# Kernel tuning notes

Measured on AMD Instinct MI355X. Metric: run time of the kernel, lower is better.

## Reference

```python
import jax, jax.numpy as jnp
import numpy as np

N_HEAD = 8


def setup_inputs() -> dict:
    key = jax.random.key(0)
    k1, k2, k3 = jax.random.split(key, 3)
    B, D, L = 4, 1024, 2048  # channels-first: (batch, feature, seq)
    q = jax.random.normal(k1, (B, D, L), dtype=jnp.float32)
    k = jax.random.normal(k2, (B, D, L), dtype=jnp.float32)
    v = jax.random.normal(k3, (B, D, L), dtype=jnp.float32)
    gamma = jnp.ones((), dtype=jnp.float32)  # nn.Parameter scalar, init 1.0
    return {"q": q, "k": k, "v": v, "gamma": gamma}


def reference(q, k, v, gamma):
    # q, k, v: (B, D, L) channels-first. Head split on feature dim (-2).
    B, Dq, Lq = q.shape
    Dv, Lk = v.shape[-2], v.shape[-1]
    h = N_HEAD
    dq = Dq // h  # per-head query/key dim
    dv = Dv // h  # per-head value dim
    qh = q.reshape(B, h, dq, Lq)
    kh = k.reshape(B, h, dq, Lk)
    vh = v.reshape(B, h, dv, Lk)
    # scale = sqrt(q.size(-2)) AFTER head split, i.e. sqrt(d_head)
    scale = 1.0 / jnp.sqrt(jnp.asarray(dq, dtype=q.dtype))
    # qk: (B, h, Lq, Lk)
    qk = jnp.einsum('bhdq,bhdl->bhql', qh, kh) * scale
    sm = jax.nn.softmax(qk, axis=-1)
    # torch: (sm.unsqueeze(-3) * v.unsqueeze(-2)).sum(-1) == contraction over Lk
    ret = jnp.einsum('bhql,bhdl->bhdq', sm, vh)  # (B, h, dv, Lq)
    ret = ret.reshape(B, Dv, Lq)  # torch: ret.view(-1, v_shape[-2], q_shape[-1])
    return gamma * ret
```

## Files before the change

kernel.cpp:

```cpp
#include <hip/hip_runtime.h>

#define SEQ 2048
#define DHEAD 128
#define BK 32
#define NBH 32

typedef __attribute__((ext_vector_type(8))) short bf16x8;
typedef __attribute__((ext_vector_type(4))) float f32x4;

__device__ __forceinline__ unsigned short f2bf(float f) {
    unsigned u = __builtin_bit_cast(unsigned, f);
    u += 0x7fffu + ((u >> 16) & 1u);
    return (unsigned short)(u >> 16);
}

__device__ __forceinline__ void gload16(const unsigned short* g, unsigned short* l) {
    __builtin_amdgcn_global_load_lds((const __attribute__((address_space(1))) void*)g,
                                     (__attribute__((address_space(3))) void*)l, 16, 0, 0);
}

__global__ __launch_bounds__(256)
void cvt_kernel(const float* __restrict__ kin, const float* __restrict__ vin,
                unsigned short* __restrict__ kout, unsigned short* __restrict__ vout) {
    const int tid = threadIdx.x;
    if (blockIdx.x < 1024) {
        __shared__ unsigned short tileT[DHEAD][66];
        const int bh = blockIdx.x & 31;
        const int l0 = (blockIdx.x >> 5) * 64;
        const float* ip = kin + (size_t)bh * DHEAD * SEQ;
        unsigned short* opx = kout + ((size_t)bh * SEQ + l0) * DHEAD;
        const int l4 = (tid & 15) * 4;
        const int dq = tid >> 4;
        for (int pass = 0; pass < 8; ++pass) {
            int d = pass * 16 + dq;
            float4 f = *(const float4*)&ip[(size_t)d * SEQ + l0 + l4];
            unsigned lo = (unsigned)f2bf(f.x) | ((unsigned)f2bf(f.y) << 16);
            unsigned hi = (unsigned)f2bf(f.z) | ((unsigned)f2bf(f.w) << 16);
            *(unsigned*)&tileT[d][l4]     = lo;
            *(unsigned*)&tileT[d][l4 + 2] = hi;
        }
        __syncthreads();
        const int lw = tid >> 2;
        const int cw = tid & 3;
        for (int j = 0; j < 4; ++j) {
            int pc = j * 4 + cw;
            int lc = pc ^ (lw & 7);
            unsigned short tmp[8];
            for (int k2 = 0; k2 < 8; ++k2) tmp[k2] = tileT[lc * 8 + k2][lw];
            *(bf16x8*)&opx[(size_t)lw * DHEAD + pc * 8] = *(bf16x8*)tmp;
        }
    } else {
        size_t f = ((size_t)(blockIdx.x - 1024) * 256 + tid) * 8;
        int bh  = (int)(f >> 18);
        int rem = (int)(f & 262143);
        int kt  = rem >> 12;
        int r2  = rem & 4095;
        int dv  = r2 >> 5;
        int e0  = r2 & 31;
        const float* src = vin + ((size_t)bh * DHEAD + dv) * SEQ + kt * BK + e0;
        float4 a = *(const float4*)src;
        float4 b = *(const float4*)(src + 4);
        unsigned short r[8] = {f2bf(a.x), f2bf(a.y), f2bf(a.z), f2bf(a.w),
                               f2bf(b.x), f2bf(b.y), f2bf(b.z), f2bf(b.w)};
        int pc = (e0 >> 3) ^ ((dv >> 1) & 3);
        size_t off = ((size_t)bh * (SEQ / BK) + kt) * (DHEAD * BK) + dv * BK + pc * 8;
        *(bf16x8*)&vout[off] = *(bf16x8*)r;
    }
}

__global__ __launch_bounds__(256, 4)
void attn_main(const float* __restrict__ q,
               const unsigned short* __restrict__ kTg,
               const unsigned short* __restrict__ vW,
               const float* __restrict__ gamma,
               float* __restrict__ out) {
    __shared__ unsigned short kS[2][BK * DHEAD];
    __shared__ unsigned short vS[2][DHEAD * BK];
    __shared__ unsigned short pS[4][16][40];

    const int tid  = threadIdx.x;
    const int wv   = tid >> 6;
    const int lane = tid & 63;
    const int c    = lane & 15;
    const int quad = lane >> 4;

    const int bh  = blockIdx.x & 31;
    const int qlb = blockIdx.x >> 5;
    const size_t base = (size_t)bh * SEQ * DHEAD;

    const float* qp = q + base;
    const unsigned short* kb = kTg + base;
    const unsigned short* vb = vW + base;
    float* op = out + base;

    const int ql0 = qlb * 64 + wv * 16;
    const float SCL = 0.08838834764831845f * 1.44269504088896340f;

    bf16x8 qf[4];
    {
        const int ql = ql0 + c;
        for (int s = 0; s < 4; ++s) {
            bf16x8 fqs;
            for (int j = 0; j < 8; ++j)
                fqs[j] = (short)f2bf(qp[(size_t)(s * 32 + quad * 8 + j) * SEQ + ql] * SCL);
            qf[s] = fqs;
        }
    }

    f32x4 accO[8];
    for (int t = 0; t < 8; ++t) accO[t] = (f32x4){0.f, 0.f, 0.f, 0.f};
    float lp[4] = {0.f, 0.f, 0.f, 0.f};

    const int ksw = c & 7;
    const int vsw = (c >> 1) & 3;

    {
        const unsigned short* kg = kb;
        gload16(kg + tid * 8,         &kS[0][tid * 8]);
        gload16(kg + (tid + 256) * 8, &kS[0][(tid + 256) * 8]);
        const unsigned short* vg = vb;
        gload16(vg + tid * 8,         &vS[0][tid * 8]);
        gload16(vg + (tid + 256) * 8, &vS[0][(tid + 256) * 8]);
    }

    for (int kt = 0; kt < SEQ / BK; ++kt) {
        const int cur = kt & 1;
        __syncthreads();

        if (kt + 1 < SEQ / BK) {
            const unsigned short* kg = kb + (size_t)(kt + 1) * (BK * DHEAD);
            gload16(kg + tid * 8,         &kS[cur ^ 1][tid * 8]);
            gload16(kg + (tid + 256) * 8, &kS[cur ^ 1][(tid + 256) * 8]);
            const unsigned short* vg = vb + (size_t)(kt + 1) * (DHEAD * BK);
            gload16(vg + tid * 8,         &vS[cur ^ 1][tid * 8]);
            gload16(vg + (tid + 256) * 8, &vS[cur ^ 1][(tid + 256) * 8]);
        }

        bf16x8 vf[8];
        for (int t = 0; t < 8; ++t)
            vf[t] = *(const bf16x8*)&vS[cur][(t * 16 + c) * BK + ((quad ^ vsw) * 8)];

        f32x4 s0 = (f32x4){0.f, 0.f, 0.f, 0.f};
        f32x4 s1 = (f32x4){0.f, 0.f, 0.f, 0.f};
        for (int s = 0; s < 4; ++s) {
            int pc = (4 * s + quad) ^ ksw;
            bf16x8 b0 = *(const bf16x8*)&kS[cur][c * DHEAD + pc * 8];
            bf16x8 b1 = *(const bf16x8*)&kS[cur][(16 + c) * DHEAD + pc * 8];
            s0 = __builtin_amdgcn_mfma_f32_16x16x32_bf16(qf[s], b0, s0, 0, 0, 0);
            s1 = __builtin_amdgcn_mfma_f32_16x16x32_bf16(qf[s], b1, s1, 0, 0, 0);
        }

        for (int r = 0; r < 4; ++r) {
            float p0 = exp2f(s0[r]);
            float p1 = exp2f(s1[r]);
            lp[r] += p0 + p1;
            pS[wv][4 * quad + r][c]      = f2bf(p0);
            pS[wv][4 * quad + r][16 + c] = f2bf(p1);
        }
        asm volatile("s_waitcnt lgkmcnt(0)" ::: "memory");

        bf16x8 bp = *(const bf16x8*)&pS[wv][c][quad * 8];
        for (int t = 0; t < 8; ++t)
            accO[t] = __builtin_amdgcn_mfma_f32_16x16x32_bf16(vf[t], bp, accO[t], 0, 0, 0);
    }

    const float gm = gamma[0];
    float L[4];
    for (int r = 0; r < 4; ++r) {
        float s = lp[r];
        s += __shfl_xor(s, 1, 16);
        s += __shfl_xor(s, 2, 16);
        s += __shfl_xor(s, 4, 16);
        s += __shfl_xor(s, 8, 16);
        L[r] = s;
    }
    int srcl = (c >> 2) << 4;
    float L0 = __shfl(L[0], srcl);
    float L1 = __shfl(L[1], srcl);
    float L2 = __shfl(L[2], srcl);
    float L3 = __shfl(L[3], srcl);
    int rsel = c & 3;
    float lsel = rsel == 0 ? L0 : rsel == 1 ? L1 : rsel == 2 ? L2 : L3;
    float sc = gm / lsel;
    int ql = ql0 + c;
    for (int t = 0; t < 8; ++t)
        for (int r = 0; r < 4; ++r)
            op[(size_t)(t * 16 + quad * 4 + r) * SEQ + ql] = accO[t][r] * sc;
}

extern "C" void kernel_launch(void* const* d_in, const int* in_sizes, int n_in,
                              void* d_out, int out_size, void* d_ws, size_t ws_size,
                              hipStream_t stream) {
    (void)in_sizes; (void)n_in; (void)out_size; (void)ws_size;
    const float* q = (const float*)d_in[0];
    const float* k = (const float*)d_in[1];
    const float* v = (const float*)d_in[2];
    const float* g = (const float*)d_in[3];
    float* out = (float*)d_out;

    const size_t PER_T = (size_t)NBH * SEQ * DHEAD;
    unsigned short* kws = (unsigned short*)d_ws;
    unsigned short* vws = kws + PER_T;

    cvt_kernel<<<dim3(1024 + 4096), dim3(256), 0, stream>>>(k, v, kws, vws);
    attn_main<<<dim3(1024), dim3(256), 0, stream>>>(q, kws, vws, g, out);
}
```

Measured before the change: 232.6 us.

## Process 64 query rows per wave to reuse K/V fragments across subtiles

Each wave now covers four 16-row query subtiles instead of one. K and V fragments are loaded from LDS once per key tile and reused across all four subtiles. The grid shrinks from 1024 to 256 blocks, and launch bounds drop to 1 block per CU to leave room for the larger register footprint (accumulators for 4x8 tiles plus Q fragments). This cuts LDS and global K/V traffic per query, but it also cuts occupancy to one wave per SIMD, which reduces latency hiding around the serial softmax-through-LDS step.

```diff
diff --git a/kernel.cpp b/kernel.cpp
--- a/kernel.cpp
+++ b/kernel.cpp
@@ -68,7 +68,7 @@
     }
 }
 
-__global__ __launch_bounds__(256, 4)
+__global__ __launch_bounds__(256, 1)
 void attn_main(const float* __restrict__ q,
                const unsigned short* __restrict__ kTg,
                const unsigned short* __restrict__ vW,
@@ -93,34 +93,36 @@
     const unsigned short* vb = vW + base;
     float* op = out + base;
 
-    const int ql0 = qlb * 64 + wv * 16;
+    const int ql0 = qlb * 256 + wv * 64;
     const float SCL = 0.08838834764831845f * 1.44269504088896340f;
 
-    bf16x8 qf[4];
-    {
-        const int ql = ql0 + c;
+    bf16x8 qf[4][4];
+    for (int rs = 0; rs < 4; ++rs) {
+        const int ql = ql0 + rs * 16 + c;
         for (int s = 0; s < 4; ++s) {
             bf16x8 fqs;
             for (int j = 0; j < 8; ++j)
                 fqs[j] = (short)f2bf(qp[(size_t)(s * 32 + quad * 8 + j) * SEQ + ql] * SCL);
-            qf[s] = fqs;
-        }
-    }
-
-    f32x4 accO[8];
-    for (int t = 0; t < 8; ++t) accO[t] = (f32x4){0.f, 0.f, 0.f, 0.f};
-    float lp[4] = {0.f, 0.f, 0.f, 0.f};
+            qf[rs][s] = fqs;
+        }
+    }
+
+    f32x4 accO[4][8];
+    for (int rs = 0; rs < 4; ++rs)
+        for (int t = 0; t < 8; ++t)
+            accO[rs][t] = (f32x4){0.f, 0.f, 0.f, 0.f};
+    float lp[4][4];
+    for (int rs = 0; rs < 4; ++rs)
+        for (int r = 0; r < 4; ++r) lp[rs][r] = 0.f;
 
     const int ksw = c & 7;
     const int vsw = (c >> 1) & 3;
 
     {
-        const unsigned short* kg = kb;
-        gload16(kg + tid * 8,         &kS[0][tid * 8]);
-        gload16(kg + (tid + 256) * 8, &kS[0][(tid + 256) * 8]);
-        const unsigned short* vg = vb;
-        gload16(vg + tid * 8,         &vS[0][tid * 8]);
-        gload16(vg + (tid + 256) * 8, &vS[0][(tid + 256) * 8]);
+        gload16(kb + tid * 8,         &kS[0][tid * 8]);
+        gload16(kb + (tid + 256) * 8, &kS[0][(tid + 256) * 8]);
+        gload16(vb + tid * 8,         &vS[0][tid * 8]);
+        gload16(vb + (tid + 256) * 8, &vS[0][(tid + 256) * 8]);
     }
 
     for (int kt = 0; kt < SEQ / BK; ++kt) {
@@ -136,56 +138,63 @@
             gload16(vg + (tid + 256) * 8, &vS[cur ^ 1][(tid + 256) * 8]);
         }
 
+        bf16x8 kf0[4], kf1[4];
+        for (int s = 0; s < 4; ++s) {
+            int pc = (4 * s + quad) ^ ksw;
+            kf0[s] = *(const bf16x8*)&kS[cur][c * DHEAD + pc * 8];
+            kf1[s] = *(const bf16x8*)&kS[cur][(16 + c) * DHEAD + pc * 8];
+        }
         bf16x8 vf[8];
         for (int t = 0; t < 8; ++t)
             vf[t] = *(const bf16x8*)&vS[cur][(t * 16 + c) * BK + ((quad ^ vsw) * 8)];
 
-        f32x4 s0 = (f32x4){0.f, 0.f, 0.f, 0.f};
-        f32x4 s1 = (f32x4){0.f, 0.f, 0.f, 0.f};
-        for (int s = 0; s < 4; ++s) {
-            int pc = (4 * s + quad) ^ ksw;
-            bf16x8 b0 = *(const bf16x8*)&kS[cur][c * DHEAD + pc * 8];
-            bf16x8 b1 = *(const bf16x8*)&kS[cur][(16 + c) * DHEAD + pc * 8];
-            s0 = __builtin_amdgcn_mfma_f32_16x16x32_bf16(qf[s], b0, s0, 0, 0, 0);
-            s1 = __builtin_amdgcn_mfma_f32_16x16x32_bf16(qf[s], b1, s1, 0, 0, 0);
-        }
-
+        for (int rs = 0; rs < 4; ++rs) {
+            f32x4 s0 = (f32x4){0.f, 0.f, 0.f, 0.f};
+            f32x4 s1 = (f32x4){0.f, 0.f, 0.f, 0.f};
+            for (int s = 0; s < 4; ++s) {
+                s0 = __builtin_amdgcn_mfma_f32_16x16x32_bf16(qf[rs][s], kf0[s], s0, 0, 0, 0);
+                s1 = __builtin_amdgcn_mfma_f32_16x16x32_bf16(qf[rs][s], kf1[s], s1, 0, 0, 0);
+            }
+
+            for (int r = 0; r < 4; ++r) {
+                float p0 = exp2f(s0[r]);
+                float p1 = exp2f(s1[r]);
+                lp[rs][r] += p0 + p1;
+                pS[wv][4 * quad + r][c]      = f2bf(p0);
+                pS[wv][4 * quad + r][16 + c] = f2bf(p1);
+            }
+            asm volatile("s_waitcnt lgkmcnt(0)" ::: "memory");
+
+            bf16x8 bp = *(const bf16x8*)&pS[wv][c][quad * 8];
+            for (int t = 0; t < 8; ++t)
+                accO[rs][t] = __builtin_amdgcn_mfma_f32_16x16x32_bf16(vf[t], bp, accO[rs][t], 0, 0, 0);
+        }
+    }
+
+    const float gm = gamma[0];
+    for (int rs = 0; rs < 4; ++rs) {
+        float L[4];
         for (int r = 0; r < 4; ++r) {
-            float p0 = exp2f(s0[r]);
-            float p1 = exp2f(s1[r]);
-            lp[r] += p0 + p1;
-            pS[wv][4 * quad + r][c]      = f2bf(p0);
-            pS[wv][4 * quad + r][16 + c] = f2bf(p1);
-        }
-        asm volatile("s_waitcnt lgkmcnt(0)" ::: "memory");
-
-        bf16x8 bp = *(const bf16x8*)&pS[wv][c][quad * 8];
+            float s = lp[rs][r];
+            s += __shfl_xor(s, 1, 16);
+            s += __shfl_xor(s, 2, 16);
+            s += __shfl_xor(s, 4, 16);
+            s += __shfl_xor(s, 8, 16);
+            L[r] = s;
+        }
+        int srcl = (c >> 2) << 4;
+        float L0 = __shfl(L[0], srcl);
+        float L1 = __shfl(L[1], srcl);
+        float L2 = __shfl(L[2], srcl);
+        float L3 = __shfl(L[3], srcl);
+        int rsel = c & 3;
+        float lsel = rsel == 0 ? L0 : rsel == 1 ? L1 : rsel == 2 ? L2 : L3;
+        float sc = gm / lsel;
+        int ql = ql0 + rs * 16 + c;
         for (int t = 0; t < 8; ++t)
-            accO[t] = __builtin_amdgcn_mfma_f32_16x16x32_bf16(vf[t], bp, accO[t], 0, 0, 0);
-    }
-
-    const float gm = gamma[0];
-    float L[4];
-    for (int r = 0; r < 4; ++r) {
-        float s = lp[r];
-        s += __shfl_xor(s, 1, 16);
-        s += __shfl_xor(s, 2, 16);
-        s += __shfl_xor(s, 4, 16);
-        s += __shfl_xor(s, 8, 16);
-        L[r] = s;
-    }
-    int srcl = (c >> 2) << 4;
-    float L0 = __shfl(L[0], srcl);
-    float L1 = __shfl(L[1], srcl);
-    float L2 = __shfl(L[2], srcl);
-    float L3 = __shfl(L[3], srcl);
-    int rsel = c & 3;
-    float lsel = rsel == 0 ? L0 : rsel == 1 ? L1 : rsel == 2 ? L2 : L3;
-    float sc = gm / lsel;
-    int ql = ql0 + c;
-    for (int t = 0; t < 8; ++t)
-        for (int r = 0; r < 4; ++r)
-            op[(size_t)(t * 16 + quad * 4 + r) * SEQ + ql] = accO[t][r] * sc;
+            for (int r = 0; r < 4; ++r)
+                op[(size_t)(t * 16 + quad * 4 + r) * SEQ + ql] = accO[rs][t][r] * sc;
+    }
 }
 
 extern "C" void kernel_launch(void* const* d_in, const int* in_sizes, int n_in,
@@ -203,5 +212,5 @@
     unsigned short* vws = kws + PER_T;
 
     cvt_kernel<<<dim3(1024 + 4096), dim3(256), 0, stream>>>(k, v, kws, vws);
-    attn_main<<<dim3(1024), dim3(256), 0, stream>>>(q, kws, vws, g, out);
-}
+    attn_main<<<dim3(256), dim3(256), 0, stream>>>(q, kws, vws, g, out);
+}
```

Result: slower. 257.8 us (+10.8%).
